# Optimization experiments

Hardware: AMD Instinct MI355X
Metric: run time of the kernel (lower is better)

The kernel has to match this reference:

```python
import jax, jax.numpy as jnp
import numpy as np

B, N, D, H, F = 16, 257, 1024, 16, 4096
HD = D // H
EPS = 1e-5
GATING_TEMP = 0.25  # gating_hyperparam for steep_sigmoid
SCALE = HD ** -0.5


def layer_norm(x, g, b):
    mu = jnp.mean(x, axis=-1, keepdims=True)
    var = jnp.mean(jnp.square(x - mu), axis=-1, keepdims=True)
    return (x - mu) * jax.lax.rsqrt(var + EPS) * g + b


def quick_gelu(x):
    return x * jax.nn.sigmoid(1.702 * x)


def setup_inputs() -> dict:
    key = jax.random.key(0)
    ks = jax.random.split(key, 24)
    s = 0.02
    inp = {
        'hidden_states': jax.random.normal(ks[0], (B, N, D), jnp.float32),
        'cached_hidden': jax.random.normal(ks[1], (B, N, D), jnp.float32),
        'cached_q': jax.random.normal(ks[2], (B, N, D), jnp.float32),
        'cached_k': jax.random.normal(ks[3], (B, N, D), jnp.float32),
        'cached_v': jax.random.normal(ks[4], (B, N, D), jnp.float32),
        'ln1_g': jnp.ones((D,), jnp.float32),
        'ln1_b': jnp.zeros((D,), jnp.float32),
        'wq': jax.random.normal(ks[5], (D, D), jnp.float32) * s,
        'bq': jnp.zeros((D,), jnp.float32),
        'wk': jax.random.normal(ks[6], (D, D), jnp.float32) * s,
        'bk': jnp.zeros((D,), jnp.float32),
        'wv': jax.random.normal(ks[7], (D, D), jnp.float32) * s,
        'bv': jnp.zeros((D,), jnp.float32),
        'wo': jax.random.normal(ks[8], (D, D), jnp.float32) * s,
        'bo': jnp.zeros((D,), jnp.float32),
        'ln2_g': jnp.ones((D,), jnp.float32),
        'ln2_b': jnp.zeros((D,), jnp.float32),
        'w1': jax.random.normal(ks[9], (D, F), jnp.float32) * s,
        'b1': jnp.zeros((F,), jnp.float32),
        'w2': jax.random.normal(ks[10], (F, D), jnp.float32) * s,
        'b2': jnp.zeros((D,), jnp.float32),
        'threshold': jnp.float32(0.5),
    }
    return inp


def reference(hidden_states, cached_hidden, cached_q, cached_k, cached_v,
              ln1_g, ln1_b, wq, bq, wk, bk, wv, bv, wo, bo,
              ln2_g, ln2_b, w1, b1, w2, b2, threshold):
    # layer_norm1 + QKV projection (layer_norm1_qkv_projection)
    h_ln = layer_norm(hidden_states, ln1_g, ln1_b)
    q = h_ln @ wq + bq
    k = h_ln @ wk + bk
    v = h_ln @ wv + bv

    # reuse module: cosine^1 similarity vs cached hidden, steep_sigmoid gating
    # against learned threshold; soft gather/scatter blend of cached states.
    num = jnp.sum(cached_hidden * hidden_states, axis=-1)           # [B,N]
    den = (jnp.linalg.norm(cached_hidden, axis=-1)
           * jnp.linalg.norm(hidden_states, axis=-1) + 1e-8)
    sim = num / den                                                 # [B,N]
    gate = jax.nn.sigmoid((sim - threshold) / GATING_TEMP)[..., None]  # [B,N,1]

    hidden = gate * cached_hidden + (1.0 - gate) * hidden_states
    q = gate * cached_q + (1.0 - gate) * q
    k = gate * cached_k + (1.0 - gate) * k
    v = gate * cached_v + (1.0 - gate) * v

    # manual bmm-softmax-bmm attention
    qh = (q * SCALE).reshape(B, N, H, HD).transpose(0, 2, 1, 3)  # [B,H,N,hd]
    kh = k.reshape(B, N, H, HD).transpose(0, 2, 1, 3)
    vh = v.reshape(B, N, H, HD).transpose(0, 2, 1, 3)
    scores = jnp.einsum('bhqd,bhkd->bhqk', qh, kh)
    probs = jax.nn.softmax(scores, axis=-1)
    attn = jnp.einsum('bhqk,bhkd->bhqd', probs, vh)
    attn = attn.transpose(0, 2, 1, 3).reshape(B, N, D)
    attn = attn @ wo + bo

    hidden = hidden + attn
    residual = hidden
    hidden = layer_norm(hidden, ln2_g, ln2_b)
    hidden = quick_gelu(hidden @ w1 + b1) @ w2 + b2
    return residual + hidden
```

## Files before the change

### kernel.cpp

```cpp
#include <hip/hip_runtime.h>
#include <hip/hip_bf16.h>
#include <stdint.h>

#define BB   16
#define SEQ  257
#define DD   1024
#define NH   16
#define HD_  64
#define FF   4096
#define MM   (BB*SEQ)
#define MPAD2 4352
#define SPAD 272
#define VPAD 288
#define SCALE_Q 0.125f

typedef __bf16 bf16x8 __attribute__((ext_vector_type(8)));
typedef float  f32x4  __attribute__((ext_vector_type(4)));
typedef unsigned short u16;

__device__ __forceinline__ u16 f2bf(float f) {
  uint32_t u = __float_as_uint(f);
  uint32_t r = (u + 0x7FFFu + ((u >> 16) & 1u)) >> 16;
  return (u16)r;
}
__device__ __forceinline__ float bf2f(u16 u) {
  return __uint_as_float(((uint32_t)u) << 16);
}
__device__ __forceinline__ void gll16(const void* g, void* l) {
  __builtin_amdgcn_global_load_lds(
      (const __attribute__((address_space(1))) void*)g,
      (__attribute__((address_space(3))) void*)l, 16, 0, 0);
}
__device__ __forceinline__ float wsum(float v) {
  #pragma unroll
  for (int o = 1; o < 64; o <<= 1) v += __shfl_xor(v, o);
  return v;
}

__global__ __launch_bounds__(256) void transpose_all(
    const float* __restrict__ wq, const float* __restrict__ wk,
    const float* __restrict__ wv, const float* __restrict__ wo,
    const float* __restrict__ w1, const float* __restrict__ w2,
    u16* __restrict__ wqkvT, u16* __restrict__ woT,
    u16* __restrict__ w1T, u16* __restrict__ w2T) {
  __shared__ float tile[64][65];
  const int bid = blockIdx.x;
  const float* src;  u16* dst;  int R, C, b;
  if (bid < 768)       { int s = bid >> 8;  b = bid & 255;
                         src = s==0?wq:(s==1?wk:wv);  dst = wqkvT + s*1024*1024;
                         R = 1024; C = 1024; }
  else if (bid < 1024) { src = wo;  dst = woT;  b = bid - 768;   R = 1024; C = 1024; }
  else if (bid < 2048) { src = w1;  dst = w1T;  b = bid - 1024;  R = 1024; C = 4096; }
  else                 { src = w2;  dst = w2T;  b = bid - 2048;  R = 4096; C = 1024; }
  const int ctiles = C >> 6;
  const int r0 = (b / ctiles) << 6, c0 = (b % ctiles) << 6;
  const int tx = threadIdx.x & 63, ty = threadIdx.x >> 6;
  #pragma unroll
  for (int it = 0; it < 16; ++it) {
    int rr = it * 4 + ty;
    tile[rr][tx] = src[(size_t)(r0 + rr) * C + c0 + tx];
  }
  __syncthreads();
  #pragma unroll
  for (int it = 0; it < 16; ++it) {
    int rr = it * 4 + ty;
    dst[(size_t)(c0 + rr) * R + r0 + tx] = f2bf(tile[tx][rr]);
  }
}

__global__ __launch_bounds__(256) void vtrans_kernel(
    const u16* __restrict__ vb, u16* __restrict__ vt) {
  __shared__ u16 tile[64][72];
  const int bh = blockIdx.x, c = blockIdx.y;
  const int tx = threadIdx.x & 63, ty = threadIdx.x >> 6;
  const u16* src = vb + (size_t)bh * SPAD * HD_;
  u16* dst = vt + (size_t)bh * HD_ * VPAD;
  #pragma unroll
  for (int it = 0; it < 16; ++it) {
    int r = it * 4 + ty;
    int nn = c * 64 + r;  int nnc = nn < SPAD ? nn : SPAD - 1;
    tile[r][tx] = src[(size_t)nnc * HD_ + tx];
  }
  __syncthreads();
  #pragma unroll
  for (int it = 0; it < 16; ++it) {
    int hd = it * 4 + ty;
    int col = c * 64 + tx;
    if (col < VPAD) dst[(size_t)hd * VPAD + col] = tile[tx][hd];
  }
}

__global__ __launch_bounds__(256) void ln1_gate_kernel(
    const float* __restrict__ h, const float* __restrict__ c,
    const float* __restrict__ g, const float* __restrict__ bta,
    const float* __restrict__ thr, u16* __restrict__ hln,
    float* __restrict__ hblend, float* __restrict__ gate) {
  int m = blockIdx.x, t = threadIdx.x, l = t & 63, w = t >> 6;
  const float4 hv = *(const float4*)(h + (size_t)m * DD + t * 4);
  const float4 cv = *(const float4*)(c + (size_t)m * DD + t * 4);
  float sh = hv.x + hv.y + hv.z + hv.w;
  float sh2 = hv.x*hv.x + hv.y*hv.y + hv.z*hv.z + hv.w*hv.w;
  float sch = hv.x*cv.x + hv.y*cv.y + hv.z*cv.z + hv.w*cv.w;
  float sc2 = cv.x*cv.x + cv.y*cv.y + cv.z*cv.z + cv.w*cv.w;
  sh = wsum(sh); sh2 = wsum(sh2); sch = wsum(sch); sc2 = wsum(sc2);
  __shared__ float red[4][4];
  if (l == 0) { red[w][0]=sh; red[w][1]=sh2; red[w][2]=sch; red[w][3]=sc2; }
  __syncthreads();
  float Sh  = red[0][0]+red[1][0]+red[2][0]+red[3][0];
  float Sh2 = red[0][1]+red[1][1]+red[2][1]+red[3][1];
  float Sch = red[0][2]+red[1][2]+red[2][2]+red[3][2];
  float Sc2 = red[0][3]+red[1][3]+red[2][3]+red[3][3];
  float mean = Sh * (1.f/DD);
  float var  = Sh2 * (1.f/DD) - mean*mean;
  float rs   = rsqrtf(var + 1e-5f);
  float sim  = Sch / (sqrtf(Sc2)*sqrtf(Sh2) + 1e-8f);
  float gv   = 1.f / (1.f + __expf(-(sim - thr[0]) * 4.0f));
  float4 gg = *(const float4*)(g + t*4);
  float4 bb = *(const float4*)(bta + t*4);
  ushort4 ob;
  ob.x = f2bf((hv.x-mean)*rs*gg.x + bb.x);
  ob.y = f2bf((hv.y-mean)*rs*gg.y + bb.y);
  ob.z = f2bf((hv.z-mean)*rs*gg.z + bb.z);
  ob.w = f2bf((hv.w-mean)*rs*gg.w + bb.w);
  *(ushort4*)(hln + (size_t)m * DD + t * 4) = ob;
  float4 hb;
  hb.x = gv*cv.x + (1.f-gv)*hv.x;  hb.y = gv*cv.y + (1.f-gv)*hv.y;
  hb.z = gv*cv.z + (1.f-gv)*hv.z;  hb.w = gv*cv.w + (1.f-gv)*hv.w;
  *(float4*)(hblend + (size_t)m * DD + t * 4) = hb;
  if (t == 0) gate[m] = gv;
}

__global__ __launch_bounds__(256) void ln2_kernel(
    const float* __restrict__ in, const float* __restrict__ g,
    const float* __restrict__ bta, u16* __restrict__ outb) {
  int m = blockIdx.x, t = threadIdx.x, l = t & 63, w = t >> 6;
  const float4 hv = *(const float4*)(in + (size_t)m * DD + t * 4);
  float sh = hv.x + hv.y + hv.z + hv.w;
  float sh2 = hv.x*hv.x + hv.y*hv.y + hv.z*hv.z + hv.w*hv.w;
  sh = wsum(sh); sh2 = wsum(sh2);
  __shared__ float red[4][2];
  if (l == 0) { red[w][0] = sh; red[w][1] = sh2; }
  __syncthreads();
  float Sh  = red[0][0]+red[1][0]+red[2][0]+red[3][0];
  float Sh2 = red[0][1]+red[1][1]+red[2][1]+red[3][1];
  float mean = Sh * (1.f/DD);
  float rs = rsqrtf(Sh2 * (1.f/DD) - mean*mean + 1e-5f);
  float4 gg = *(const float4*)(g + t*4);
  float4 bb = *(const float4*)(bta + t*4);
  ushort4 ob;
  ob.x = f2bf((hv.x-mean)*rs*gg.x + bb.x);
  ob.y = f2bf((hv.y-mean)*rs*gg.y + bb.y);
  ob.z = f2bf((hv.z-mean)*rs*gg.z + bb.z);
  ob.w = f2bf((hv.w-mean)*rs*gg.w + bb.w);
  *(ushort4*)(outb + (size_t)m * DD + t * 4) = ob;
}

template<int EPI>
__global__ __launch_bounds__(256, 3) void gemm_bt(
    const u16* __restrict__ A, const u16* __restrict__ Bt,
    int Kstride, int Kiter,
    const float* __restrict__ bias,
    const float* __restrict__ gate,
    const float* __restrict__ c0, const float* __restrict__ c1, const float* __restrict__ c2,
    const float* __restrict__ bq, const float* __restrict__ bk, const float* __restrict__ bv,
    u16* __restrict__ qb, u16* __restrict__ kb, u16* __restrict__ vb,
    const float* __restrict__ addsrc, float* __restrict__ outf,
    u16* __restrict__ outb, u16* __restrict__ partb) {
  const int tid = threadIdx.x, w = tid >> 6, l = tid & 63, lr = l & 15, lh = l >> 4;
  const int Mt = gridDim.x;
  const int f = blockIdx.y * Mt + blockIdx.x;
  const int nwg = Mt * gridDim.y;
  const int q8 = nwg >> 3, r8 = nwg & 7, xcd = f & 7, lin = f >> 3;
  const int swz = (xcd < r8 ? xcd * (q8 + 1) : r8 * (q8 + 1) + (xcd - r8) * q8) + lin;
  const int m0 = (swz % Mt) * 128, n0 = (swz / Mt) * 128;
  const int kBase = blockIdx.z * Kiter;
  const int wm = w >> 1, wn = w & 1;
  __shared__ u16 sA[3][4096], sB[3][4096];
  f32x4 acc[4][4];
  f32x4 zero = {0.f, 0.f, 0.f, 0.f};
  #pragma unroll
  for (int i = 0; i < 4; ++i)
    #pragma unroll
    for (int j = 0; j < 4; ++j) acc[i][j] = zero;

  const int rS = tid >> 2;
  const int srcC = (((tid & 3) ^ ((tid >> 3) & 3)) * 8);
  const u16* gA = A  + (size_t)(m0 + rS) * Kstride + kBase + srcC;
  const u16* gB = Bt + (size_t)(n0 + rS) * Kstride + kBase + srcC;
  const size_t rStep = (size_t)64 * Kstride;

  const int sL = (lr >> 1) & 3;
  const int coff = ((lh ^ sL) & 3) * 8;
  const int rdA = (wm*64 + lr) * 32 + coff;
  const int rdB = (wn*64 + lr) * 32 + coff;

  #define STAGE(S_, T_) do { \
    const int _ko = (T_) << 5; \
    gll16(gA + _ko,         &sA[S_][0]    + tid*8); \
    gll16(gA + _ko + rStep, &sA[S_][2048] + tid*8); \
    gll16(gB + _ko,         &sB[S_][0]    + tid*8); \
    gll16(gB + _ko + rStep, &sB[S_][2048] + tid*8); \
  } while(0)

  const int nt = Kiter >> 5;
  STAGE(0, 0);
  STAGE(1, 1);
  #pragma unroll 1
  for (int t = 0; t < nt; ++t) {
    const int sc = t % 3;
    __builtin_amdgcn_s_barrier();
    if (t + 2 < nt) {
      STAGE((t + 2) % 3, t + 2);
      asm volatile("s_waitcnt vmcnt(8)" ::: "memory");
    } else if (t + 1 < nt) {
      asm volatile("s_waitcnt vmcnt(4)" ::: "memory");
    } else {
      asm volatile("s_waitcnt vmcnt(0)" ::: "memory");
    }
    __builtin_amdgcn_sched_barrier(0);
    __builtin_amdgcn_s_barrier();
    __builtin_amdgcn_sched_barrier(0);
    bf16x8 af[4], bfr[4];
    #pragma unroll
    for (int mi = 0; mi < 4; ++mi)
      af[mi] = *(const bf16x8*)&sA[sc][rdA + mi*512];
    #pragma unroll
    for (int ni = 0; ni < 4; ++ni)
      bfr[ni] = *(const bf16x8*)&sB[sc][rdB + ni*512];
    #pragma unroll
    for (int mi = 0; mi < 4; ++mi)
      #pragma unroll
      for (int ni = 0; ni < 4; ++ni)
        acc[mi][ni] = __builtin_amdgcn_mfma_f32_16x16x32_bf16(af[mi], bfr[ni], acc[mi][ni], 0, 0, 0);
  }
  #undef STAGE

  if constexpr (EPI == 0) {
    const int which = n0 >> 10;
    const float* cb = which==0 ? bq : (which==1 ? bk : bv);
    const float* cp = which==0 ? c0 : (which==1 ? c1 : c2);
    u16* dst = which==0 ? qb : (which==1 ? kb : vb);
    const float scl = which==0 ? SCALE_Q : 1.0f;
    #pragma unroll
    for (int mi = 0; mi < 4; ++mi) {
      #pragma unroll
      for (int r = 0; r < 4; ++r) {
        const int row = m0 + wm*64 + mi*16 + lh*4 + r;
        if (row < MM) {
          const float gv = gate[row];
          const int bidx = row / SEQ, nn = row - bidx * SEQ;
          #pragma unroll
          for (int ni = 0; ni < 4; ++ni) {
            const int col = n0 + wn*64 + ni*16 + lr;
            const int d = col & 1023, hd = d & 63, hh = d >> 6;
            const float lin2 = acc[mi][ni][r] + cb[d];
            const float val = (gv * cp[(size_t)row*DD + d] + (1.f - gv) * lin2) * scl;
            dst[((size_t)(bidx*NH + hh)*SPAD + nn)*HD_ + hd] = f2bf(val);
          }
        }
      }
    }
  } else if constexpr (EPI == 1) {
    #pragma unroll
    for (int mi = 0; mi < 4; ++mi)
      #pragma unroll
      for (int r = 0; r < 4; ++r) {
        const int row = m0 + wm*64 + mi*16 + lh*4 + r;
        if (row < MM) {
          #pragma unroll
          for (int ni = 0; ni < 4; ++ni) {
            const int col = n0 + wn*64 + ni*16 + lr;
            outf[(size_t)row*DD + col] = acc[mi][ni][r] + bias[col] + addsrc[(size_t)row*DD + col];
          }
        }
      }
  } else if constexpr (EPI == 2) {
    #pragma unroll
    for (int mi = 0; mi < 4; ++mi)
      #pragma unroll
      for (int r = 0; r < 4; ++r) {
        const int row = m0 + wm*64 + mi*16 + lh*4 + r;
        if (row < MM) {
          #pragma unroll
          for (int ni = 0; ni < 4; ++ni) {
            const int col = n0 + wn*64 + ni*16 + lr;
            const float x = acc[mi][ni][r] + bias[col];
            const float s = 1.f / (1.f + __expf(-1.702f * x));
            outb[(size_t)row*FF + col] = f2bf(x * s);
          }
        }
      }
  } else {
    u16* pp = partb + (size_t)blockIdx.z * ((size_t)MPAD2 * 1024);
    #pragma unroll
    for (int mi = 0; mi < 4; ++mi)
      #pragma unroll
      for (int r = 0; r < 4; ++r) {
        const int row = m0 + wm*64 + mi*16 + lh*4 + r;
        if (row < MM) {
          #pragma unroll
          for (int ni = 0; ni < 4; ++ni) {
            const int col = n0 + wn*64 + ni*16 + lr;
            pp[(size_t)row*1024 + col] = f2bf(acc[mi][ni][r]);
          }
        }
      }
  }
}

__global__ __launch_bounds__(256) void reduce_mlp2(
    const u16* __restrict__ parts, const float* __restrict__ bias,
    const float* __restrict__ resid, float* __restrict__ out) {
  const size_t PS = (size_t)MPAD2 * 1024;
  const int row = blockIdx.x, t = threadIdx.x, c = t * 4;
  const size_t base = (size_t)row * 1024 + c;
  float4 r = *(const float4*)(resid + base);
  float4 b = *(const float4*)(bias + c);
  float o0 = r.x + b.x, o1 = r.y + b.y, o2 = r.z + b.z, o3 = r.w + b.w;
  #pragma unroll
  for (int p = 0; p < 2; ++p) {
    ushort4 u = *(const ushort4*)(parts + p*PS + base);
    o0 += bf2f(u.x);  o1 += bf2f(u.y);  o2 += bf2f(u.z);  o3 += bf2f(u.w);
  }
  float4 o;  o.x = o0;  o.y = o1;  o.z = o2;  o.w = o3;
  *(float4*)(out + base) = o;
}

__global__ __launch_bounds__(256) void attn_kernel(
    const u16* __restrict__ qb, const u16* __restrict__ kb,
    const u16* __restrict__ vt, u16* __restrict__ attn_out) {
  __shared__ u16 P[64 * 296];
  const int bh = blockIdx.x, b = bh >> 4, hh = bh & 15;
  const int q0 = blockIdx.y * 64;
  const int tid = threadIdx.x, w = tid >> 6, l = tid & 63, lr = l & 15, lh = l >> 4;
  const u16* qp = qb + (size_t)bh * SPAD * HD_;
  const u16* kp = kb + (size_t)bh * SPAD * HD_;
  const u16* vp = vt + (size_t)bh * HD_ * VPAD;

  const int qr = q0 + w*16 + lr;
  const int qrc = qr < 271 ? qr : 271;
  bf16x8 aq0 = *(const bf16x8*)(qp + (size_t)qrc*HD_ + lh*8);
  bf16x8 aq1 = *(const bf16x8*)(qp + (size_t)qrc*HD_ + 32 + lh*8);

  f32x4 st[18];
  f32x4 zero = {0.f,0.f,0.f,0.f};
  #pragma unroll
  for (int t = 0; t < 18; ++t) st[t] = zero;
  #pragma unroll
  for (int t = 0; t < 18; ++t) {
    int key = t*16 + lr;  int keyc = key < 271 ? key : 271;
    bf16x8 b0 = *(const bf16x8*)(kp + (size_t)keyc*HD_ + lh*8);
    bf16x8 b1 = *(const bf16x8*)(kp + (size_t)keyc*HD_ + 32 + lh*8);
    st[t] = __builtin_amdgcn_mfma_f32_16x16x32_bf16(aq0, b0, st[t], 0, 0, 0);
    st[t] = __builtin_amdgcn_mfma_f32_16x16x32_bf16(aq1, b1, st[t], 0, 0, 0);
  }
  #pragma unroll
  for (int t = 0; t < 18; ++t) {
    int key = t*16 + lr;
    if (key >= SEQ) { st[t][0]=-1e30f; st[t][1]=-1e30f; st[t][2]=-1e30f; st[t][3]=-1e30f; }
  }
  float mr[4], sr[4];
  #pragma unroll
  for (int r = 0; r < 4; ++r) {
    float m = st[0][r];
    #pragma unroll
    for (int t = 1; t < 18; ++t) m = fmaxf(m, st[t][r]);
    m = fmaxf(m, __shfl_xor(m, 1));  m = fmaxf(m, __shfl_xor(m, 2));
    m = fmaxf(m, __shfl_xor(m, 4));  m = fmaxf(m, __shfl_xor(m, 8));
    mr[r] = m;  sr[r] = 0.f;
  }
  #pragma unroll
  for (int t = 0; t < 18; ++t)
    #pragma unroll
    for (int r = 0; r < 4; ++r) {
      float p = __expf(st[t][r] - mr[r]);
      st[t][r] = p;  sr[r] += p;
    }
  #pragma unroll
  for (int r = 0; r < 4; ++r) {
    sr[r] += __shfl_xor(sr[r], 1);  sr[r] += __shfl_xor(sr[r], 2);
    sr[r] += __shfl_xor(sr[r], 4);  sr[r] += __shfl_xor(sr[r], 8);
  }
  #pragma unroll
  for (int t = 0; t < 18; ++t)
    #pragma unroll
    for (int r = 0; r < 4; ++r)
      P[(w*16 + lh*4 + r)*296 + t*16 + lr] = f2bf(st[t][r]);
  __syncthreads();

  f32x4 o[4];
  #pragma unroll
  for (int ni = 0; ni < 4; ++ni) o[ni] = zero;
  #pragma unroll
  for (int ks = 0; ks < 9; ++ks) {
    bf16x8 pa = *(const bf16x8*)&P[(w*16 + lr)*296 + ks*32 + lh*8];
    #pragma unroll
    for (int ni = 0; ni < 4; ++ni) {
      bf16x8 bv_ = *(const bf16x8*)(vp + (size_t)(ni*16 + lr)*VPAD + ks*32 + lh*8);
      o[ni] = __builtin_amdgcn_mfma_f32_16x16x32_bf16(pa, bv_, o[ni], 0, 0, 0);
    }
  }
  #pragma unroll
  for (int r = 0; r < 4; ++r) {
    const int qrow = q0 + w*16 + lh*4 + r;
    if (qrow < SEQ) {
      const float inv = 1.f / sr[r];
      #pragma unroll
      for (int ni = 0; ni < 4; ++ni)
        attn_out[(size_t)(b*SEQ + qrow)*DD + hh*HD_ + ni*16 + lr] = f2bf(o[ni][r] * inv);
    }
  }
}

extern "C" void kernel_launch(void* const* d_in, const int* in_sizes, int n_in,
                              void* d_out, int out_size, void* d_ws, size_t ws_size,
                              hipStream_t stream) {
  (void)in_sizes; (void)n_in; (void)out_size; (void)ws_size;
  const float* hidden   = (const float*)d_in[0];
  const float* cached_h = (const float*)d_in[1];
  const float* cached_q = (const float*)d_in[2];
  const float* cached_k = (const float*)d_in[3];
  const float* cached_v = (const float*)d_in[4];
  const float* ln1_g = (const float*)d_in[5];
  const float* ln1_b = (const float*)d_in[6];
  const float* wq = (const float*)d_in[7];
  const float* bq = (const float*)d_in[8];
  const float* wk = (const float*)d_in[9];
  const float* bk = (const float*)d_in[10];
  const float* wv = (const float*)d_in[11];
  const float* bv = (const float*)d_in[12];
  const float* wo = (const float*)d_in[13];
  const float* bo = (const float*)d_in[14];
  const float* ln2_g = (const float*)d_in[15];
  const float* ln2_b = (const float*)d_in[16];
  const float* w1 = (const float*)d_in[17];
  const float* b1 = (const float*)d_in[18];
  const float* w2 = (const float*)d_in[19];
  const float* b2 = (const float*)d_in[20];
  const float* thr = (const float*)d_in[21];
  float* out = (float*)d_out;

  char* ws = (char*)d_ws;
  size_t off = 0;
  auto alloc = [&](size_t bytes) {
    void* p = ws + off;  off += (bytes + 255) & ~(size_t)255;  return p;
  };
  u16*   wqkvT  = (u16*)alloc(3072ull * 1024 * 2);
  u16*   woT    = (u16*)alloc(1024ull * 1024 * 2);
  u16*   w1T    = (u16*)alloc(4096ull * 1024 * 2);
  u16*   w2T    = (u16*)alloc(1024ull * 4096 * 2);
  float* gate   = (float*)alloc((size_t)MPAD2 * 4);
  float* resid2 = (float*)alloc((size_t)MPAD2 * DD * 4);
  u16*   regA   = (u16*)alloc((size_t)MPAD2 * DD * 2);
  u16 *hln = regA, *attn_o = regA, *ln2out = regA;
  const size_t QKV_B  = (size_t)256 * SPAD * HD_ * 2;
  const size_t VT_B   = (size_t)256 * HD_ * VPAD * 2;
  const size_t PART_B = (size_t)MPAD2 * 1024 * 2;
  const size_t partsOff = 3*QKV_B + VT_B;
  char*  regB   = (char*)alloc(partsOff + 2*PART_B);
  u16*   qbuf   = (u16*)regB;
  u16*   kbuf   = (u16*)(regB + QKV_B);
  u16*   vbuf   = (u16*)(regB + 2*QKV_B);
  u16*   vtb    = (u16*)(regB + 3*QKV_B);
  float* hblend = (float*)(regB + partsOff);
  u16*   mid    = (u16*)regB;
  u16*   parts  = (u16*)(regB + partsOff);

  dim3 blk(256);
  transpose_all<<<dim3(3072), blk, 0, stream>>>(wq, wk, wv, wo, w1, w2,
                                                wqkvT, woT, w1T, w2T);

  ln1_gate_kernel<<<dim3(MM), blk, 0, stream>>>(hidden, cached_h, ln1_g, ln1_b, thr,
                                                hln, hblend, gate);

  gemm_bt<0><<<dim3(33, 24), blk, 0, stream>>>(hln, wqkvT, 1024, 1024, nullptr,
      gate, cached_q, cached_k, cached_v, bq, bk, bv, qbuf, kbuf, vbuf,
      nullptr, nullptr, nullptr, nullptr);

  vtrans_kernel<<<dim3(256, 5), blk, 0, stream>>>(vbuf, vtb);
  attn_kernel<<<dim3(256, 5), blk, 0, stream>>>(qbuf, kbuf, vtb, attn_o);

  gemm_bt<1><<<dim3(33, 8), blk, 0, stream>>>(attn_o, woT, 1024, 1024, bo,
      nullptr, nullptr, nullptr, nullptr, nullptr, nullptr, nullptr,
      nullptr, nullptr, nullptr, hblend, resid2, nullptr, nullptr);

  ln2_kernel<<<dim3(MM), blk, 0, stream>>>(resid2, ln2_g, ln2_b, ln2out);

  gemm_bt<2><<<dim3(33, 32), blk, 0, stream>>>(ln2out, w1T, 1024, 1024, b1,
      nullptr, nullptr, nullptr, nullptr, nullptr, nullptr, nullptr,
      nullptr, nullptr, nullptr, nullptr, nullptr, mid, nullptr);

  gemm_bt<3><<<dim3(33, 8, 2), blk, 0, stream>>>(mid, w2T, 4096, 2048, nullptr,
      nullptr, nullptr, nullptr, nullptr, nullptr, nullptr, nullptr,
      nullptr, nullptr, nullptr, nullptr, nullptr, nullptr, parts);

  reduce_mlp2<<<dim3(MM), blk, 0, stream>>>(parts, b2, resid2, out);
}
```

Baseline: 313.1 us.

## Split-K the output projection and MLP2 GEMMs, double-buffer the GEMM for occupancy

```diff
diff --git a/kernel.cpp b/kernel.cpp
--- a/kernel.cpp
+++ b/kernel.cpp
@@ -156,7 +156,7 @@
 }
 
 template<int EPI>
-__global__ __launch_bounds__(256, 3) void gemm_bt(
+__global__ __launch_bounds__(256, 5) void gemm_bt(
     const u16* __restrict__ A, const u16* __restrict__ Bt,
     int Kstride, int Kiter,
     const float* __restrict__ bias,
@@ -164,8 +164,7 @@
     const float* __restrict__ c0, const float* __restrict__ c1, const float* __restrict__ c2,
     const float* __restrict__ bq, const float* __restrict__ bk, const float* __restrict__ bv,
     u16* __restrict__ qb, u16* __restrict__ kb, u16* __restrict__ vb,
-    const float* __restrict__ addsrc, float* __restrict__ outf,
-    u16* __restrict__ outb, u16* __restrict__ partb) {
+    u16* __restrict__ outb, u16* __restrict__ partb, float* __restrict__ partf) {
   const int tid = threadIdx.x, w = tid >> 6, l = tid & 63, lr = l & 15, lh = l >> 4;
   const int Mt = gridDim.x;
   const int f = blockIdx.y * Mt + blockIdx.x;
@@ -175,7 +174,7 @@
   const int m0 = (swz % Mt) * 128, n0 = (swz / Mt) * 128;
   const int kBase = blockIdx.z * Kiter;
   const int wm = w >> 1, wn = w & 1;
-  __shared__ u16 sA[3][4096], sB[3][4096];
+  __shared__ u16 sA[2][4096], sB[2][4096];
   f32x4 acc[4][4];
   f32x4 zero = {0.f, 0.f, 0.f, 0.f};
   #pragma unroll
@@ -204,29 +203,18 @@
 
   const int nt = Kiter >> 5;
   STAGE(0, 0);
-  STAGE(1, 1);
   #pragma unroll 1
   for (int t = 0; t < nt; ++t) {
-    const int sc = t % 3;
-    __builtin_amdgcn_s_barrier();
-    if (t + 2 < nt) {
-      STAGE((t + 2) % 3, t + 2);
-      asm volatile("s_waitcnt vmcnt(8)" ::: "memory");
-    } else if (t + 1 < nt) {
-      asm volatile("s_waitcnt vmcnt(4)" ::: "memory");
-    } else {
-      asm volatile("s_waitcnt vmcnt(0)" ::: "memory");
-    }
-    __builtin_amdgcn_sched_barrier(0);
-    __builtin_amdgcn_s_barrier();
-    __builtin_amdgcn_sched_barrier(0);
+    const int cur = t & 1;
+    __syncthreads();
+    if (t + 1 < nt) STAGE(cur ^ 1, t + 1);
     bf16x8 af[4], bfr[4];
     #pragma unroll
     for (int mi = 0; mi < 4; ++mi)
-      af[mi] = *(const bf16x8*)&sA[sc][rdA + mi*512];
+      af[mi] = *(const bf16x8*)&sA[cur][rdA + mi*512];
     #pragma unroll
     for (int ni = 0; ni < 4; ++ni)
-      bfr[ni] = *(const bf16x8*)&sB[sc][rdB + ni*512];
+      bfr[ni] = *(const bf16x8*)&sB[cur][rdB + ni*512];
     #pragma unroll
     for (int mi = 0; mi < 4; ++mi)
       #pragma unroll
@@ -260,20 +248,6 @@
         }
       }
     }
-  } else if constexpr (EPI == 1) {
-    #pragma unroll
-    for (int mi = 0; mi < 4; ++mi)
-      #pragma unroll
-      for (int r = 0; r < 4; ++r) {
-        const int row = m0 + wm*64 + mi*16 + lh*4 + r;
-        if (row < MM) {
-          #pragma unroll
-          for (int ni = 0; ni < 4; ++ni) {
-            const int col = n0 + wn*64 + ni*16 + lr;
-            outf[(size_t)row*DD + col] = acc[mi][ni][r] + bias[col] + addsrc[(size_t)row*DD + col];
-          }
-        }
-      }
   } else if constexpr (EPI == 2) {
     #pragma unroll
     for (int mi = 0; mi < 4; ++mi)
@@ -290,7 +264,7 @@
           }
         }
       }
-  } else {
+  } else if constexpr (EPI == 3) {
     u16* pp = partb + (size_t)blockIdx.z * ((size_t)MPAD2 * 1024);
     #pragma unroll
     for (int mi = 0; mi < 4; ++mi)
@@ -305,7 +279,40 @@
           }
         }
       }
-  }
+  } else {
+    float* pp = partf + (size_t)blockIdx.z * ((size_t)MPAD2 * 1024);
+    #pragma unroll
+    for (int mi = 0; mi < 4; ++mi)
+      #pragma unroll
+      for (int r = 0; r < 4; ++r) {
+        const int row = m0 + wm*64 + mi*16 + lh*4 + r;
+        if (row < MM) {
+          #pragma unroll
+          for (int ni = 0; ni < 4; ++ni) {
+            const int col = n0 + wn*64 + ni*16 + lr;
+            pp[(size_t)row*1024 + col] = acc[mi][ni][r];
+          }
+        }
+      }
+  }
+}
+
+__global__ __launch_bounds__(256) void reduce_oproj(
+    const float* __restrict__ parts, const float* __restrict__ bias,
+    const float* __restrict__ hblend, float* __restrict__ resid2) {
+  const size_t PS = (size_t)MPAD2 * 1024;
+  const int row = blockIdx.x, t = threadIdx.x, c = t * 4;
+  const size_t base = (size_t)row * 1024 + c;
+  float4 p0 = *(const float4*)(parts + base);
+  float4 p1 = *(const float4*)(parts + PS + base);
+  float4 hb = *(const float4*)(hblend + base);
+  float4 b  = *(const float4*)(bias + c);
+  float4 o;
+  o.x = p0.x + p1.x + b.x + hb.x;
+  o.y = p0.y + p1.y + b.y + hb.y;
+  o.z = p0.z + p1.z + b.z + hb.z;
+  o.w = p0.w + p1.w + b.w + hb.w;
+  *(float4*)(resid2 + base) = o;
 }
 
 __global__ __launch_bounds__(256) void reduce_mlp2(
@@ -318,7 +325,7 @@
   float4 b = *(const float4*)(bias + c);
   float o0 = r.x + b.x, o1 = r.y + b.y, o2 = r.z + b.z, o3 = r.w + b.w;
   #pragma unroll
-  for (int p = 0; p < 2; ++p) {
+  for (int p = 0; p < 4; ++p) {
     ushort4 u = *(const ushort4*)(parts + p*PS + base);
     o0 += bf2f(u.x);  o1 += bf2f(u.y);  o2 += bf2f(u.z);  o3 += bf2f(u.w);
   }
@@ -456,14 +463,17 @@
   const size_t QKV_B  = (size_t)256 * SPAD * HD_ * 2;
   const size_t VT_B   = (size_t)256 * HD_ * VPAD * 2;
   const size_t PART_B = (size_t)MPAD2 * 1024 * 2;
-  const size_t partsOff = 3*QKV_B + VT_B;
-  char*  regB   = (char*)alloc(partsOff + 2*PART_B);
+  const size_t PARTF_B= (size_t)MPAD2 * 1024 * 4;
+  const size_t frontB = 3*QKV_B + VT_B;
+  const size_t partsOff = frontB;
+  char*  regB   = (char*)alloc(partsOff + 4*PART_B);
   u16*   qbuf   = (u16*)regB;
   u16*   kbuf   = (u16*)(regB + QKV_B);
   u16*   vbuf   = (u16*)(regB + 2*QKV_B);
   u16*   vtb    = (u16*)(regB + 3*QKV_B);
+  float* opart  = (float*)regB;
+  u16*   mid    = (u16*)regB;
   float* hblend = (float*)(regB + partsOff);
-  u16*   mid    = (u16*)regB;
   u16*   parts  = (u16*)(regB + partsOff);
 
   dim3 blk(256);
@@ -475,24 +485,25 @@
 
   gemm_bt<0><<<dim3(33, 24), blk, 0, stream>>>(hln, wqkvT, 1024, 1024, nullptr,
       gate, cached_q, cached_k, cached_v, bq, bk, bv, qbuf, kbuf, vbuf,
-      nullptr, nullptr, nullptr, nullptr);
+      nullptr, nullptr, nullptr);
 
   vtrans_kernel<<<dim3(256, 5), blk, 0, stream>>>(vbuf, vtb);
   attn_kernel<<<dim3(256, 5), blk, 0, stream>>>(qbuf, kbuf, vtb, attn_o);
 
-  gemm_bt<1><<<dim3(33, 8), blk, 0, stream>>>(attn_o, woT, 1024, 1024, bo,
+  gemm_bt<4><<<dim3(33, 8, 2), blk, 0, stream>>>(attn_o, woT, 1024, 512, nullptr,
       nullptr, nullptr, nullptr, nullptr, nullptr, nullptr, nullptr,
-      nullptr, nullptr, nullptr, hblend, resid2, nullptr, nullptr);
+      nullptr, nullptr, nullptr, nullptr, nullptr, opart);
+  reduce_oproj<<<dim3(MM), blk, 0, stream>>>(opart, bo, hblend, resid2);
 
   ln2_kernel<<<dim3(MM), blk, 0, stream>>>(resid2, ln2_g, ln2_b, ln2out);
 
   gemm_bt<2><<<dim3(33, 32), blk, 0, stream>>>(ln2out, w1T, 1024, 1024, b1,
       nullptr, nullptr, nullptr, nullptr, nullptr, nullptr, nullptr,
-      nullptr, nullptr, nullptr, nullptr, nullptr, mid, nullptr);
-
-  gemm_bt<3><<<dim3(33, 8, 2), blk, 0, stream>>>(mid, w2T, 4096, 2048, nullptr,
+      nullptr, nullptr, nullptr, mid, nullptr, nullptr);
+
+  gemm_bt<3><<<dim3(33, 8, 4), blk, 0, stream>>>(mid, w2T, 4096, 1024, nullptr,
       nullptr, nullptr, nullptr, nullptr, nullptr, nullptr, nullptr,
-      nullptr, nullptr, nullptr, nullptr, nullptr, nullptr, parts);
+      nullptr, nullptr, nullptr, nullptr, parts, nullptr);
 
   reduce_mlp2<<<dim3(MM), blk, 0, stream>>>(parts, b2, resid2, out);
 }
```

Result: slower. 336.8 us (+7.6%).

## Merge weight transpose with LN1 gating; use two-stage GEMM LDS pipeline

Applied to the files above, without the earlier changes.

```diff
diff --git a/kernel.cpp b/kernel.cpp
--- a/kernel.cpp
+++ b/kernel.cpp
@@ -37,34 +37,75 @@
   return v;
 }
 
-__global__ __launch_bounds__(256) void transpose_all(
+__global__ __launch_bounds__(256) void prologue_kernel(
     const float* __restrict__ wq, const float* __restrict__ wk,
     const float* __restrict__ wv, const float* __restrict__ wo,
     const float* __restrict__ w1, const float* __restrict__ w2,
     u16* __restrict__ wqkvT, u16* __restrict__ woT,
-    u16* __restrict__ w1T, u16* __restrict__ w2T) {
+    u16* __restrict__ w1T, u16* __restrict__ w2T,
+    const float* __restrict__ h, const float* __restrict__ c,
+    const float* __restrict__ g, const float* __restrict__ bta,
+    const float* __restrict__ thr, u16* __restrict__ hln,
+    float* __restrict__ hblend, float* __restrict__ gate) {
   __shared__ float tile[64][65];
+  __shared__ float red[4][4];
   const int bid = blockIdx.x;
-  const float* src;  u16* dst;  int R, C, b;
-  if (bid < 768)       { int s = bid >> 8;  b = bid & 255;
-                         src = s==0?wq:(s==1?wk:wv);  dst = wqkvT + s*1024*1024;
-                         R = 1024; C = 1024; }
-  else if (bid < 1024) { src = wo;  dst = woT;  b = bid - 768;   R = 1024; C = 1024; }
-  else if (bid < 2048) { src = w1;  dst = w1T;  b = bid - 1024;  R = 1024; C = 4096; }
-  else                 { src = w2;  dst = w2T;  b = bid - 2048;  R = 4096; C = 1024; }
-  const int ctiles = C >> 6;
-  const int r0 = (b / ctiles) << 6, c0 = (b % ctiles) << 6;
-  const int tx = threadIdx.x & 63, ty = threadIdx.x >> 6;
-  #pragma unroll
-  for (int it = 0; it < 16; ++it) {
-    int rr = it * 4 + ty;
-    tile[rr][tx] = src[(size_t)(r0 + rr) * C + c0 + tx];
-  }
-  __syncthreads();
-  #pragma unroll
-  for (int it = 0; it < 16; ++it) {
-    int rr = it * 4 + ty;
-    dst[(size_t)(c0 + rr) * R + r0 + tx] = f2bf(tile[tx][rr]);
+  if (bid < 3072) {
+    const float* src;  u16* dst;  int R, C, b;
+    if (bid < 768)       { int s = bid >> 8;  b = bid & 255;
+                           src = s==0?wq:(s==1?wk:wv);  dst = wqkvT + s*1024*1024;
+                           R = 1024; C = 1024; }
+    else if (bid < 1024) { src = wo;  dst = woT;  b = bid - 768;   R = 1024; C = 1024; }
+    else if (bid < 2048) { src = w1;  dst = w1T;  b = bid - 1024;  R = 1024; C = 4096; }
+    else                 { src = w2;  dst = w2T;  b = bid - 2048;  R = 4096; C = 1024; }
+    const int ctiles = C >> 6;
+    const int r0 = (b / ctiles) << 6, c0 = (b % ctiles) << 6;
+    const int tx = threadIdx.x & 63, ty = threadIdx.x >> 6;
+    #pragma unroll
+    for (int it = 0; it < 16; ++it) {
+      int rr = it * 4 + ty;
+      tile[rr][tx] = src[(size_t)(r0 + rr) * C + c0 + tx];
+    }
+    __syncthreads();
+    #pragma unroll
+    for (int it = 0; it < 16; ++it) {
+      int rr = it * 4 + ty;
+      dst[(size_t)(c0 + rr) * R + r0 + tx] = f2bf(tile[tx][rr]);
+    }
+  } else {
+    const int m = bid - 3072;
+    const int t = threadIdx.x, l = t & 63, w = t >> 6;
+    const float4 hv = *(const float4*)(h + (size_t)m * DD + t * 4);
+    const float4 cv = *(const float4*)(c + (size_t)m * DD + t * 4);
+    float sh = hv.x + hv.y + hv.z + hv.w;
+    float sh2 = hv.x*hv.x + hv.y*hv.y + hv.z*hv.z + hv.w*hv.w;
+    float sch = hv.x*cv.x + hv.y*cv.y + hv.z*cv.z + hv.w*cv.w;
+    float sc2 = cv.x*cv.x + cv.y*cv.y + cv.z*cv.z + cv.w*cv.w;
+    sh = wsum(sh); sh2 = wsum(sh2); sch = wsum(sch); sc2 = wsum(sc2);
+    if (l == 0) { red[w][0]=sh; red[w][1]=sh2; red[w][2]=sch; red[w][3]=sc2; }
+    __syncthreads();
+    float Sh  = red[0][0]+red[1][0]+red[2][0]+red[3][0];
+    float Sh2 = red[0][1]+red[1][1]+red[2][1]+red[3][1];
+    float Sch = red[0][2]+red[1][2]+red[2][2]+red[3][2];
+    float Sc2 = red[0][3]+red[1][3]+red[2][3]+red[3][3];
+    float mean = Sh * (1.f/DD);
+    float var  = Sh2 * (1.f/DD) - mean*mean;
+    float rs   = rsqrtf(var + 1e-5f);
+    float sim  = Sch / (sqrtf(Sc2)*sqrtf(Sh2) + 1e-8f);
+    float gv   = 1.f / (1.f + __expf(-(sim - thr[0]) * 4.0f));
+    float4 gg = *(const float4*)(g + t*4);
+    float4 bb = *(const float4*)(bta + t*4);
+    ushort4 ob;
+    ob.x = f2bf((hv.x-mean)*rs*gg.x + bb.x);
+    ob.y = f2bf((hv.y-mean)*rs*gg.y + bb.y);
+    ob.z = f2bf((hv.z-mean)*rs*gg.z + bb.z);
+    ob.w = f2bf((hv.w-mean)*rs*gg.w + bb.w);
+    *(ushort4*)(hln + (size_t)m * DD + t * 4) = ob;
+    float4 hb;
+    hb.x = gv*cv.x + (1.f-gv)*hv.x;  hb.y = gv*cv.y + (1.f-gv)*hv.y;
+    hb.z = gv*cv.z + (1.f-gv)*hv.z;  hb.w = gv*cv.w + (1.f-gv)*hv.w;
+    *(float4*)(hblend + (size_t)m * DD + t * 4) = hb;
+    if (t == 0) gate[m] = gv;
   }
 }
 
@@ -88,46 +129,6 @@
     int col = c * 64 + tx;
     if (col < VPAD) dst[(size_t)hd * VPAD + col] = tile[tx][hd];
   }
-}
-
-__global__ __launch_bounds__(256) void ln1_gate_kernel(
-    const float* __restrict__ h, const float* __restrict__ c,
-    const float* __restrict__ g, const float* __restrict__ bta,
-    const float* __restrict__ thr, u16* __restrict__ hln,
-    float* __restrict__ hblend, float* __restrict__ gate) {
-  int m = blockIdx.x, t = threadIdx.x, l = t & 63, w = t >> 6;
-  const float4 hv = *(const float4*)(h + (size_t)m * DD + t * 4);
-  const float4 cv = *(const float4*)(c + (size_t)m * DD + t * 4);
-  float sh = hv.x + hv.y + hv.z + hv.w;
-  float sh2 = hv.x*hv.x + hv.y*hv.y + hv.z*hv.z + hv.w*hv.w;
-  float sch = hv.x*cv.x + hv.y*cv.y + hv.z*cv.z + hv.w*cv.w;
-  float sc2 = cv.x*cv.x + cv.y*cv.y + cv.z*cv.z + cv.w*cv.w;
-  sh = wsum(sh); sh2 = wsum(sh2); sch = wsum(sch); sc2 = wsum(sc2);
-  __shared__ float red[4][4];
-  if (l == 0) { red[w][0]=sh; red[w][1]=sh2; red[w][2]=sch; red[w][3]=sc2; }
-  __syncthreads();
-  float Sh  = red[0][0]+red[1][0]+red[2][0]+red[3][0];
-  float Sh2 = red[0][1]+red[1][1]+red[2][1]+red[3][1];
-  float Sch = red[0][2]+red[1][2]+red[2][2]+red[3][2];
-  float Sc2 = red[0][3]+red[1][3]+red[2][3]+red[3][3];
-  float mean = Sh * (1.f/DD);
-  float var  = Sh2 * (1.f/DD) - mean*mean;
-  float rs   = rsqrtf(var + 1e-5f);
-  float sim  = Sch / (sqrtf(Sc2)*sqrtf(Sh2) + 1e-8f);
-  float gv   = 1.f / (1.f + __expf(-(sim - thr[0]) * 4.0f));
-  float4 gg = *(const float4*)(g + t*4);
-  float4 bb = *(const float4*)(bta + t*4);
-  ushort4 ob;
-  ob.x = f2bf((hv.x-mean)*rs*gg.x + bb.x);
-  ob.y = f2bf((hv.y-mean)*rs*gg.y + bb.y);
-  ob.z = f2bf((hv.z-mean)*rs*gg.z + bb.z);
-  ob.w = f2bf((hv.w-mean)*rs*gg.w + bb.w);
-  *(ushort4*)(hln + (size_t)m * DD + t * 4) = ob;
-  float4 hb;
-  hb.x = gv*cv.x + (1.f-gv)*hv.x;  hb.y = gv*cv.y + (1.f-gv)*hv.y;
-  hb.z = gv*cv.z + (1.f-gv)*hv.z;  hb.w = gv*cv.w + (1.f-gv)*hv.w;
-  *(float4*)(hblend + (size_t)m * DD + t * 4) = hb;
-  if (t == 0) gate[m] = gv;
 }
 
 __global__ __launch_bounds__(256) void ln2_kernel(
@@ -156,7 +157,7 @@
 }
 
 template<int EPI>
-__global__ __launch_bounds__(256, 3) void gemm_bt(
+__global__ __launch_bounds__(256) void gemm_bt(
     const u16* __restrict__ A, const u16* __restrict__ Bt,
     int Kstride, int Kiter,
     const float* __restrict__ bias,
@@ -170,12 +171,11 @@
   const int Mt = gridDim.x;
   const int f = blockIdx.y * Mt + blockIdx.x;
   const int nwg = Mt * gridDim.y;
-  const int q8 = nwg >> 3, r8 = nwg & 7, xcd = f & 7, lin = f >> 3;
-  const int swz = (xcd < r8 ? xcd * (q8 + 1) : r8 * (q8 + 1) + (xcd - r8) * q8) + lin;
+  const int swz = (f & 7) * (nwg >> 3) + (f >> 3);
   const int m0 = (swz % Mt) * 128, n0 = (swz / Mt) * 128;
   const int kBase = blockIdx.z * Kiter;
   const int wm = w >> 1, wn = w & 1;
-  __shared__ u16 sA[3][4096], sB[3][4096];
+  __shared__ u16 sA[2][4096], sB[2][4096];
   f32x4 acc[4][4];
   f32x4 zero = {0.f, 0.f, 0.f, 0.f};
   #pragma unroll
@@ -204,29 +204,18 @@
 
   const int nt = Kiter >> 5;
   STAGE(0, 0);
-  STAGE(1, 1);
   #pragma unroll 1
   for (int t = 0; t < nt; ++t) {
-    const int sc = t % 3;
-    __builtin_amdgcn_s_barrier();
-    if (t + 2 < nt) {
-      STAGE((t + 2) % 3, t + 2);
-      asm volatile("s_waitcnt vmcnt(8)" ::: "memory");
-    } else if (t + 1 < nt) {
-      asm volatile("s_waitcnt vmcnt(4)" ::: "memory");
-    } else {
-      asm volatile("s_waitcnt vmcnt(0)" ::: "memory");
-    }
-    __builtin_amdgcn_sched_barrier(0);
-    __builtin_amdgcn_s_barrier();
-    __builtin_amdgcn_sched_barrier(0);
+    const int cur = t & 1;
+    __syncthreads();
+    if (t + 1 < nt) STAGE(cur ^ 1, t + 1);
     bf16x8 af[4], bfr[4];
     #pragma unroll
     for (int mi = 0; mi < 4; ++mi)
-      af[mi] = *(const bf16x8*)&sA[sc][rdA + mi*512];
+      af[mi] = *(const bf16x8*)&sA[cur][rdA + mi*512];
     #pragma unroll
     for (int ni = 0; ni < 4; ++ni)
-      bfr[ni] = *(const bf16x8*)&sB[sc][rdB + ni*512];
+      bfr[ni] = *(const bf16x8*)&sB[cur][rdB + ni*512];
     #pragma unroll
     for (int mi = 0; mi < 4; ++mi)
       #pragma unroll
@@ -467,11 +456,9 @@
   u16*   parts  = (u16*)(regB + partsOff);
 
   dim3 blk(256);
-  transpose_all<<<dim3(3072), blk, 0, stream>>>(wq, wk, wv, wo, w1, w2,
-                                                wqkvT, woT, w1T, w2T);
-
-  ln1_gate_kernel<<<dim3(MM), blk, 0, stream>>>(hidden, cached_h, ln1_g, ln1_b, thr,
-                                                hln, hblend, gate);
+  prologue_kernel<<<dim3(3072 + MM), blk, 0, stream>>>(
+      wq, wk, wv, wo, w1, w2, wqkvT, woT, w1T, w2T,
+      hidden, cached_h, ln1_g, ln1_b, thr, hln, hblend, gate);
 
   gemm_bt<0><<<dim3(33, 24), blk, 0, stream>>>(hln, wqkvT, 1024, 1024, nullptr,
       gate, cached_q, cached_k, cached_v, bq, bk, bv, qbuf, kbuf, vbuf,
```

Result: faster. 306.3 us (-2.2%).
